# Kernel optimization log

Hardware: AMD Instinct MI355X
Metric: run time of the kernel (lower is better)

Reference implementation:

```python
import jax, jax.numpy as jnp
import numpy as np
import math

SEQ = 45000
FEAT = 30
DEPTH, HEADS, DK, MLP, C = 4, 4, 32, 512, 32
MAXSEQ = 512


def pos_embed_table():
    # Enformer-style basis functions over distances [-SEQ+1, SEQ-1]
    d = jnp.arange(-SEQ + 1, SEQ, dtype=jnp.float32)
    a = jnp.abs(d)[:, None]
    nb = FEAT // 6  # basis per class (exponential / central-mask / gamma)
    # exponential decay
    hl = 2.0 ** jnp.linspace(3.0, math.log(SEQ) / math.log(2.0), nb)
    e1 = jnp.exp(-math.log(2.0) / hl[None, :] * a)
    # central mask
    cw = 2.0 ** jnp.arange(1, nb + 1, dtype=jnp.float32) - 1.0
    e2 = (cw[None, :] > a).astype(jnp.float32)
    # gamma pdf
    stddev = SEQ / (2 * nb)
    start_mean = SEQ / nb
    mean = jnp.linspace(start_mean, float(SEQ), nb)
    conc = (mean / stddev) ** 2
    rate = mean / stddev ** 2
    logp = jax.scipy.special.xlogy(conc - 1.0, a) - rate * a
    logz = jax.scipy.special.gammaln(conc) - conc * jnp.log(rate)
    p = jnp.exp(logp - logz) + 1e-8
    e3 = p / jnp.max(p)
    e = jnp.concatenate([e1, e2, e3], axis=-1)
    return jnp.concatenate([e, jnp.sign(d)[:, None] * e], axis=-1)  # [2*SEQ-1, FEAT]


def layernorm(x, g, b, eps=1e-5):
    mu = jnp.mean(x, axis=-1, keepdims=True)
    var = jnp.var(x, axis=-1, keepdims=True)
    return (x - mu) * jax.lax.rsqrt(var + eps) * g + b


def setup_inputs() -> dict:
    key = jax.random.key(0)
    ks = jax.random.split(key, 16)
    B, L = 2, SEQ
    HD = HEADS * DK
    s = 0.02
    return {
        "x_skip": jax.random.normal(ks[0], (B, C, L), jnp.float32),
        "attention": jax.random.uniform(ks[1], (B, 3, L), jnp.float32),
        "ln1_g": jnp.ones((DEPTH, C), jnp.float32),
        "ln1_b": jnp.zeros((DEPTH, C), jnp.float32),
        "Wq": jax.random.normal(ks[2], (DEPTH, C, HD), jnp.float32) * s,
        "Wk": jax.random.normal(ks[3], (DEPTH, C, HD), jnp.float32) * s,
        "Wv": jax.random.normal(ks[4], (DEPTH, C, HD), jnp.float32) * s,
        "Wrel": jax.random.normal(ks[5], (DEPTH, FEAT, HD), jnp.float32) * s,
        "rcb": jax.random.normal(ks[6], (DEPTH, HEADS, DK), jnp.float32),
        "rpb": jax.random.normal(ks[7], (DEPTH, HEADS, DK), jnp.float32),
        "Wo": jax.random.normal(ks[8], (DEPTH, HD, C), jnp.float32) * s,
        "bo": jnp.zeros((DEPTH, C), jnp.float32),
        "ln2_g": jnp.ones((DEPTH, C), jnp.float32),
        "ln2_b": jnp.zeros((DEPTH, C), jnp.float32),
        "W1": jax.random.normal(ks[9], (DEPTH, C, MLP), jnp.float32) * s,
        "b1": jnp.zeros((DEPTH, MLP), jnp.float32),
        "W2": jax.random.normal(ks[10], (DEPTH, MLP, C), jnp.float32) * s,
        "b2": jnp.zeros((DEPTH, C), jnp.float32),
    }


def reference(x_skip, attention, ln1_g, ln1_b, Wq, Wk, Wv, Wrel, rcb, rpb, Wo, bo, ln2_g, ln2_b, W1, b1, W2, b2):
    B, Cc, L = x_skip.shape
    half = MAXSEQ // 2
    x_emb = jnp.swapaxes(x_skip, 1, 2)  # [B, L, C]
    # top splice sites by acceptor / donor score
    acc = jnp.argsort(-attention[:, 1, :], axis=1)[:, :half]
    don = jnp.argsort(-attention[:, 2, :], axis=1)[:, :half]
    idx = jnp.sort(jnp.concatenate([acc, don], axis=1), axis=1)  # [B, n]
    n = idx.shape[1]
    diff = idx[:, :, None] - idx[:, None, :] + SEQ - 1  # [B, n, n]
    positions = pos_embed_table()[diff]  # [B, n, n, FEAT]
    emb = jnp.take_along_axis(x_emb, idx[:, :, None], axis=1)  # [B, n, C]
    scale = DK ** -0.5
    for l in range(DEPTH):
        h = layernorm(emb, ln1_g[l], ln1_b[l])
        q = (h @ Wq[l]).reshape(B, n, HEADS, DK).transpose(0, 2, 1, 3) * scale
        k = (h @ Wk[l]).reshape(B, n, HEADS, DK).transpose(0, 2, 1, 3)
        v = (h @ Wv[l]).reshape(B, n, HEADS, DK).transpose(0, 2, 1, 3)
        content = jnp.einsum('bhid,bhjd->bhij', q + rcb[l][None, :, None, :], k)
        rel_k = (positions @ Wrel[l]).reshape(B, n, n, HEADS, DK)  # b i j h d
        rel = jnp.einsum('bhid,bijhd->bhij', q + rpb[l][None, :, None, :], rel_k)
        attn_w = jax.nn.softmax(content + rel, axis=-1)
        o = jnp.einsum('bhij,bhjd->bhid', attn_w, v)
        o = o.transpose(0, 2, 1, 3).reshape(B, n, HEADS * DK)
        emb = emb + o @ Wo[l] + bo[l]
        h2 = layernorm(emb, ln2_g[l], ln2_b[l])
        emb = emb + jax.nn.gelu(h2 @ W1[l] + b1[l], approximate=False) @ W2[l] + b2[l]
    out = jnp.zeros_like(x_emb).at[jnp.arange(B)[:, None], idx].set(emb)
    return jnp.swapaxes(out, 1, 2)  # [B, C, L]
```

## Files before the change

kernel.cpp:

```cpp
#include <hip/hip_runtime.h>
#include <math.h>

#define SEQL   45000
#define NBAT   2
#define CCH    32
#define NSEL   512
#define NHEAD  4
#define DKD    32
#define HDD    128
#define MLPD   512
#define CDCAP  2048
#define TKB    32
#define ETB    176

__device__ __forceinline__ unsigned short f2bf(float x) {
  unsigned u = __float_as_uint(x);
  u = (u + 0x7fffu + ((u >> 16) & 1u)) >> 16;
  return (unsigned short)u;
}
#define BFL(u) __uint_as_float((u) << 16)
#define BFH(u) __uint_as_float((u) & 0xffff0000u)
#define U8F(w, s) ((float)(((w) >> (s)) & 0xffu))

__global__ __launch_bounds__(256) void prep_kernel(const float* __restrict__ att,
                                                   unsigned char* __restrict__ E,
                                                   int* __restrict__ hist,
                                                   float* __restrict__ out) {
  {
    int nthr = gridDim.x * 256;
    int gt = blockIdx.x * 256 + threadIdx.x;
    float4 z4 = make_float4(0.f, 0.f, 0.f, 0.f);
    float4* o4 = (float4*)out;
    for (int i = gt; i < NBAT * CCH * SEQL / 4; i += nthr) o4[i] = z4;
  }
  if (blockIdx.x < ETB) {
    int a = blockIdx.x * 256 + threadIdx.x;
    if (a >= SEQL) return;
    float ad = (float)a;
    float outv[16];
    float log2S = log2f((float)SEQL);
    #pragma unroll
    for (int k = 0; k < 5; ++k) {
      float hl = exp2f(3.0f + (float)k * (log2S - 3.0f) * 0.25f);
      outv[k] = exp2f(-ad / hl);
    }
    const int cw[5] = {1, 3, 7, 15, 31};
    #pragma unroll
    for (int k = 0; k < 5; ++k) outv[5 + k] = (a < cw[k]) ? 1.0f : 0.0f;
    float pmax = 0.0f;
    float pk[5];
    #pragma unroll
    for (int k = 0; k < 5; ++k) {
      float mean = 9000.0f * (float)(k + 1);
      float sd = 4500.0f;
      float cc = (mean / sd) * (mean / sd);
      float rr = mean / (sd * sd);
      float logz = lgammaf(cc) - cc * logf(rr);
      float pp;
      if (a == 0) pp = 1e-8f;
      else pp = expf((cc - 1.0f) * logf(ad) - rr * ad - logz) + 1e-8f;
      pk[k] = pp;
      float mstar = (cc - 1.0f) / rr;
      float m0 = floorf(mstar), m1 = m0 + 1.0f;
      if (m1 > (float)(SEQL - 1)) m1 = (float)(SEQL - 1);
      float p0 = expf((cc - 1.0f) * logf(m0) - rr * m0 - logz) + 1e-8f;
      float p1 = expf((cc - 1.0f) * logf(m1) - rr * m1 - logz) + 1e-8f;
      pmax = fmaxf(pmax, fmaxf(p0, p1));
    }
    #pragma unroll
    for (int k = 0; k < 5; ++k) outv[10 + k] = pk[k] / pmax;
    outv[15] = 0.0f;
    unsigned by[16];
    #pragma unroll
    for (int k = 0; k < 15; ++k)
      by[k] = (unsigned)(fminf(fmaxf(outv[k], 0.f), 1.f) * 255.f + 0.5f);
    by[15] = 0u;
    uint4 o;
    o.x = by[0]  | (by[1]  << 8) | (by[2]  << 16) | (by[3]  << 24);
    o.y = by[4]  | (by[5]  << 8) | (by[6]  << 16) | (by[7]  << 24);
    o.z = by[8]  | (by[9]  << 8) | (by[10] << 16) | (by[11] << 24);
    o.w = by[12] | (by[13] << 8) | (by[14] << 16);
    *(uint4*)(E + (size_t)a * 16) = o;
  } else {
    int bid = blockIdx.x - ETB;
    int ch4 = bid / TKB;
    int blk = bid % TKB;
    int b = ch4 >> 1, ch = ch4 & 1;
    const float* row = att + ((size_t)b * 3 + 1 + ch) * SEQL;
    int* h = hist + (size_t)ch4 * 65536;
    int per = (SEQL + TKB - 1) / TKB;
    int lo = blk * per;
    int hi = lo + per; if (hi > SEQL) hi = SEQL;
    for (int i = lo + threadIdx.x; i < hi; i += 256)
      atomicAdd(&h[__float_as_uint(row[i]) >> 16], 1);
  }
}

__global__ __launch_bounds__(256) void topk_collect_kernel(
    const float* __restrict__ att, const int* __restrict__ hist,
    unsigned long long* __restrict__ cand, int* __restrict__ cnt) {
  __shared__ int s_scan[256];
  __shared__ int s_aux[2];
  int tid = threadIdx.x;
  int ch4 = blockIdx.x / TKB;
  int blk = blockIdx.x % TKB;
  const int* h = hist + (size_t)ch4 * 65536;
  {
    int base = tid * 256;
    int sum = 0;
    for (int i = 0; i < 64; ++i) {
      int4 v = ((const int4*)(h + base))[i];
      sum += v.x + v.y + v.z + v.w;
    }
    s_scan[tid] = sum;
  }
  __syncthreads();
  for (int d = 1; d < 256; d <<= 1) {
    int v = s_scan[tid] + ((tid + d < 256) ? s_scan[tid + d] : 0);
    __syncthreads();
    s_scan[tid] = v;
    __syncthreads();
  }
  {
    int sufEx = (tid == 255) ? 0 : s_scan[tid + 1];
    if (s_scan[tid] >= 256 && sufEx < 256) { s_aux[0] = tid; s_aux[1] = 256 - sufEx; }
  }
  __syncthreads();
  int chunk = s_aux[0], want = s_aux[1];
  s_scan[tid] = h[chunk * 256 + tid];
  __syncthreads();
  for (int d = 1; d < 256; d <<= 1) {
    int v = s_scan[tid] + ((tid + d < 256) ? s_scan[tid + d] : 0);
    __syncthreads();
    s_scan[tid] = v;
    __syncthreads();
  }
  {
    int sufEx2 = (tid == 255) ? 0 : s_scan[tid + 1];
    if (s_scan[tid] >= want && sufEx2 < want) s_aux[0] = chunk * 256 + tid;
  }
  __syncthreads();
  unsigned T16 = (unsigned)s_aux[0];
  int b = ch4 >> 1, ch = ch4 & 1;
  const float* row = att + ((size_t)b * 3 + 1 + ch) * SEQL;
  int per = (SEQL + TKB - 1) / TKB;
  int lo = blk * per;
  int hi = lo + per; if (hi > SEQL) hi = SEQL;
  for (int i = lo + tid; i < hi; i += 256) {
    unsigned key = __float_as_uint(row[i]);
    if ((key >> 16) >= T16) {
      int p = atomicAdd(&cnt[ch4], 1);
      if (p < CDCAP)
        cand[(size_t)ch4 * CDCAP + p] =
            ((unsigned long long)key << 32) | (unsigned)(~(unsigned)i);
    }
  }
}

__global__ __launch_bounds__(1024) void topk_sort_kernel(
    const unsigned long long* __restrict__ cand, const int* __restrict__ cnt,
    unsigned* __restrict__ chsel) {
  __shared__ unsigned long long sc[CDCAP];
  int ch4 = blockIdx.x, t = threadIdx.x;
  int n = cnt[ch4]; if (n > CDCAP) n = CDCAP;
  int P = 256;
  while (P < n) P <<= 1;
  for (int i = t; i < P; i += 1024)
    sc[i] = (i < n) ? cand[(size_t)ch4 * CDCAP + i] : 0ull;
  __syncthreads();
  for (int k = 2; k <= P; k <<= 1) {
    for (int j = k >> 1; j > 0; j >>= 1) {
      for (int i = t; i < P; i += 1024) {
        int ixj = i ^ j;
        if (ixj > i) {
          unsigned long long va = sc[i], vb2 = sc[ixj];
          bool up = ((i & k) == 0);
          if ((va < vb2) == up) { sc[i] = vb2; sc[ixj] = va; }
        }
      }
      __syncthreads();
    }
  }
  if (t < 256)
    chsel[(size_t)ch4 * 256 + t] = ~(unsigned)(sc[t] & 0xFFFFFFFFull);
}

__global__ __launch_bounds__(512) void topk_merge_kernel(const unsigned* __restrict__ chsel,
                                                         int* __restrict__ idx) {
  __shared__ int m[512];
  int b = blockIdx.x, tid = threadIdx.x;
  m[tid] = (int)chsel[(size_t)b * 512 + tid];
  __syncthreads();
  for (int k = 2; k <= 512; k <<= 1) {
    for (int j = k >> 1; j > 0; j >>= 1) {
      int ixj = tid ^ j;
      if (ixj > tid) {
        int va = m[tid], vb2 = m[ixj];
        bool up = ((tid & k) == 0);
        if ((va > vb2) == up) { m[tid] = vb2; m[ixj] = va; }
      }
      __syncthreads();
    }
  }
  idx[b * 512 + tid] = m[tid];
}

__global__ __launch_bounds__(128) void gqkv0_kernel(
    const float* __restrict__ x, const int* __restrict__ idx,
    const float* __restrict__ ln_g, const float* __restrict__ ln_b,
    const float* __restrict__ Wq, const float* __restrict__ Wk,
    const float* __restrict__ Wv, const float* __restrict__ Wrel,
    const float* __restrict__ rcb, const float* __restrict__ rpb,
    float* __restrict__ emb, float* __restrict__ qc,
    unsigned short* __restrict__ kbT, unsigned short* __restrict__ vT,
    float* __restrict__ wb) {
  __shared__ float qs[128];
  const int l = 0;
  int hd = threadIdx.x;
  int hh = hd >> 5, d = hd & 31;
  int row = blockIdx.x;
  int b = row >> 9, ii = row & 511;
  int li = idx[b * NSEL + ii];
  float h[32];
  float mu = 0.f;
  #pragma unroll
  for (int c = 0; c < 32; ++c) {
    h[c] = x[((size_t)b * CCH + c) * SEQL + li];
    mu += h[c];
  }
  if (hd < 32) emb[(size_t)row * CCH + hd] = h[hd];
  mu *= (1.0f / 32.0f);
  float var = 0.f;
  #pragma unroll
  for (int c = 0; c < 32; ++c) { float dd0 = h[c] - mu; var += dd0 * dd0; }
  var *= (1.0f / 32.0f);
  float rstd = rsqrtf(var + 1e-5f);
  const float* g = ln_g + l * CCH;
  const float* bb = ln_b + l * CCH;
  #pragma unroll
  for (int c = 0; c < 32; ++c) h[c] = (h[c] - mu) * rstd * g[c] + bb[c];
  const float* wq = Wq + (size_t)l * CCH * HDD + hd;
  const float* wk = Wk + (size_t)l * CCH * HDD + hd;
  const float* wv = Wv + (size_t)l * CCH * HDD + hd;
  float q = 0.f, kk = 0.f, vv = 0.f;
  #pragma unroll
  for (int c = 0; c < 32; ++c) {
    q += h[c] * wq[c * HDD];
    kk += h[c] * wk[c * HDD];
    vv += h[c] * wv[c * HDD];
  }
  q *= 0.17677669529663687f;
  qs[hd] = q;
  qc[(size_t)row * HDD + hd] = q + rcb[(l * NHEAD + hh) * DKD + d];
  size_t tpos = ((size_t)(b * 4 + hh) * 4 + (d >> 3)) * 4096 + (size_t)ii * 8 + (d & 7);
  kbT[tpos] = f2bf(kk);
  vT[tpos]  = f2bf(vv);
  __syncthreads();
  if (hd < 120) {
    int h2 = hd / 30, f = hd % 30;
    const float* wr = Wrel + ((size_t)l * 30 + f) * HDD + h2 * DKD;
    const float* rp = rpb + (l * NHEAD + h2) * DKD;
    const float* qsh = qs + h2 * DKD;
    float acc = 0.f;
    #pragma unroll
    for (int dd = 0; dd < 32; ++dd) acc += (qsh[dd] + rp[dd]) * wr[dd];
    wb[((size_t)row * NHEAD + h2) * 32 + f] = acc;
  }
}

__global__ __launch_bounds__(256, 4) void layer_kernel(
    const float* __restrict__ qc, const unsigned short* __restrict__ kbT,
    const unsigned short* __restrict__ vT, const float* __restrict__ wbuf,
    const unsigned char* __restrict__ E, const int* __restrict__ idx,
    const float* __restrict__ Wo, const float* __restrict__ bo,
    const float* __restrict__ ln2_g, const float* __restrict__ ln2_b,
    const float* __restrict__ W1, const float* __restrict__ b1,
    const float* __restrict__ W2, const float* __restrict__ b2,
    const float* __restrict__ ln1_g, const float* __restrict__ ln1_b,
    const float* __restrict__ Wq, const float* __restrict__ Wk,
    const float* __restrict__ Wv, const float* __restrict__ Wrel,
    const float* __restrict__ rcb, const float* __restrict__ rpb,
    float* __restrict__ emb, float* __restrict__ qcN,
    unsigned short* __restrict__ kbTN, unsigned short* __restrict__ vTN,
    float* __restrict__ wbN, float* __restrict__ out, int layer) {
  __shared__ float es[16 * 512];
  __shared__ float obs[128];
  __shared__ float part[8][32];
  __shared__ float res[32];
  __shared__ float hln[32];
  __shared__ float fin[32];
  __shared__ float a1s[MLPD];
  __shared__ float qs[128];
  int bid = blockIdx.x;
  int b = bid >> 9;
  int i = bid & 511;
  int tid = threadIdx.x;
  int pos = idx[b * NSEL + i];
  #pragma unroll
  for (int rep = 0; rep < 2; ++rep) {
    int j = tid + rep * 256;
    int dj = pos - idx[b * NSEL + j];
    int a = dj < 0 ? -dj : dj;
    uint4 e = *(const uint4*)(E + (size_t)a * 16);
    es[0  * 512 + j] = U8F(e.x, 0);
    es[1  * 512 + j] = U8F(e.x, 8);
    es[2  * 512 + j] = U8F(e.x, 16);
    es[3  * 512 + j] = U8F(e.x, 24);
    es[4  * 512 + j] = U8F(e.y, 0);
    es[5  * 512 + j] = U8F(e.y, 8);
    es[6  * 512 + j] = U8F(e.y, 16);
    es[7  * 512 + j] = U8F(e.y, 24);
    es[8  * 512 + j] = U8F(e.z, 0);
    es[9  * 512 + j] = U8F(e.z, 8);
    es[10 * 512 + j] = U8F(e.z, 16);
    es[11 * 512 + j] = U8F(e.z, 24);
    es[12 * 512 + j] = U8F(e.w, 0);
    es[13 * 512 + j] = U8F(e.w, 8);
    es[14 * 512 + j] = U8F(e.w, 16);
    es[15 * 512 + j] = dj > 0 ? 1.f : (dj < 0 ? -1.f : 0.f);
  }
  __syncthreads();
  {
    int h = tid >> 6, ln = tid & 63;
    const float* qrow = qc + (size_t)(b * NSEL + i) * HDD + h * DKD;
    float q[32];
    #pragma unroll
    for (int d4 = 0; d4 < 8; ++d4) {
      float4 qv = *(const float4*)(qrow + d4 * 4);
      q[d4 * 4 + 0] = qv.x; q[d4 * 4 + 1] = qv.y;
      q[d4 * 4 + 2] = qv.z; q[d4 * 4 + 3] = qv.w;
    }
    const float* wrow = wbuf + ((size_t)(b * NSEL + i) * NHEAD + h) * 32;
    float w0[15], w1[15];
    #pragma unroll
    for (int f = 0; f < 15; ++f) {
      w0[f] = wrow[f] * (1.0f / 255.0f);
      w1[f] = wrow[15 + f] * (1.0f / 255.0f);
    }
    const uint4* kb4 = (const uint4*)kbT + (size_t)(b * 4 + h) * 4 * 512;
    const uint4* vb4 = (const uint4*)vT + (size_t)(b * 4 + h) * 4 * 512;
    float lg[8];
    #pragma unroll
    for (int u = 0; u < 8; ++u) {
      int j = u * 64 + ln;
      float cacc = 0.f;
      #pragma unroll
      for (int dp = 0; dp < 4; ++dp) {
        uint4 kv = kb4[dp * 512 + j];
        cacc += q[dp * 8 + 0] * BFL(kv.x) + q[dp * 8 + 1] * BFH(kv.x)
              + q[dp * 8 + 2] * BFL(kv.y) + q[dp * 8 + 3] * BFH(kv.y)
              + q[dp * 8 + 4] * BFL(kv.z) + q[dp * 8 + 5] * BFH(kv.z)
              + q[dp * 8 + 6] * BFL(kv.w) + q[dp * 8 + 7] * BFH(kv.w);
      }
      float r0 = 0.f, r1 = 0.f;
      #pragma unroll
      for (int f = 0; f < 15; ++f) {
        float ef = es[f * 512 + j];
        r0 += ef * w0[f];
        r1 += ef * w1[f];
      }
      lg[u] = cacc + r0 + es[15 * 512 + j] * r1;
    }
    float m = lg[0];
    #pragma unroll
    for (int u = 1; u < 8; ++u) m = fmaxf(m, lg[u]);
    #pragma unroll
    for (int s = 1; s < 64; s <<= 1) m = fmaxf(m, __shfl_xor(m, s));
    float ssum = 0.f;
    #pragma unroll
    for (int u = 0; u < 8; ++u) { lg[u] = __expf(lg[u] - m); ssum += lg[u]; }
    #pragma unroll
    for (int s = 1; s < 64; s <<= 1) ssum += __shfl_xor(ssum, s);
    float invs = 1.0f / ssum;
    #pragma unroll
    for (int dp = 0; dp < 4; ++dp) {
      float acc[8] = {0.f, 0.f, 0.f, 0.f, 0.f, 0.f, 0.f, 0.f};
      #pragma unroll
      for (int u = 0; u < 8; ++u) {
        uint4 vv = vb4[dp * 512 + u * 64 + ln];
        float p = lg[u];
        acc[0] += p * BFL(vv.x); acc[1] += p * BFH(vv.x);
        acc[2] += p * BFL(vv.y); acc[3] += p * BFH(vv.y);
        acc[4] += p * BFL(vv.z); acc[5] += p * BFH(vv.z);
        acc[6] += p * BFL(vv.w); acc[7] += p * BFH(vv.w);
      }
      #pragma unroll
      for (int s = 1; s < 8; s <<= 1) {
        #pragma unroll
        for (int t = 0; t < 8; ++t) acc[t] += __shfl_xor(acc[t], s);
      }
      int sel = ln & 7;
      float y = acc[0];
      #pragma unroll
      for (int t = 1; t < 8; ++t) y = (sel == t) ? acc[t] : y;
      #pragma unroll
      for (int s = 8; s < 64; s <<= 1) y += __shfl_xor(y, s);
      if (ln < 8) obs[h * DKD + dp * 8 + ln] = y * invs;
    }
  }
  __syncthreads();
  int c = tid & 31, seg = tid >> 5;
  {
    const float* wo = Wo + (size_t)layer * HDD * CCH + c;
    float pacc = 0.f;
    #pragma unroll
    for (int k = 0; k < 16; ++k) {
      int kk = seg * 16 + k;
      pacc += obs[kk] * wo[kk * CCH];
    }
    part[seg][c] = pacc;
  }
  __syncthreads();
  if (tid < 32) {
    float s = bo[layer * CCH + tid] + emb[(size_t)bid * CCH + tid];
    #pragma unroll
    for (int sg = 0; sg < 8; ++sg) s += part[sg][tid];
    res[tid] = s;
  }
  __syncthreads();
  if (tid < 32) {
    float mu = 0.f, s2 = 0.f;
    #pragma unroll
    for (int c2 = 0; c2 < 32; ++c2) { float v = res[c2]; mu += v; s2 += v * v; }
    mu *= (1.0f / 32.0f);
    float var = s2 * (1.0f / 32.0f) - mu * mu;
    float rstd = rsqrtf(var + 1e-5f);
    hln[tid] = (res[tid] - mu) * rstd * ln2_g[layer * CCH + tid] + ln2_b[layer * CCH + tid];
  }
  __syncthreads();
  {
    const float* w1 = W1 + (size_t)layer * CCH * MLPD;
    float accA = b1[layer * MLPD + tid];
    float accB = b1[layer * MLPD + tid + 256];
    for (int c2 = 0; c2 < 32; ++c2) {
      float hv = hln[c2];
      accA += hv * w1[c2 * MLPD + tid];
      accB += hv * w1[c2 * MLPD + tid + 256];
    }
    a1s[tid]       = 0.5f * accA * (1.0f + erff(accA * 0.70710678118654752f));
    a1s[tid + 256] = 0.5f * accB * (1.0f + erff(accB * 0.70710678118654752f));
  }
  __syncthreads();
  {
    const float* w2 = W2 + (size_t)layer * MLPD * CCH;
    float acc2 = 0.f;
    #pragma unroll 4
    for (int mi = 0; mi < 64; ++mi) {
      int m = seg * 64 + mi;
      acc2 += a1s[m] * w2[m * CCH + c];
    }
    __syncthreads();
    part[seg][c] = acc2;
  }
  __syncthreads();
  if (tid < 32) {
    float s = b2[layer * CCH + tid] + res[tid];
    #pragma unroll
    for (int sg = 0; sg < 8; ++sg) s += part[sg][tid];
    fin[tid] = s;
    if (layer < 3) emb[(size_t)bid * CCH + tid] = s;
  }
  __syncthreads();
  if (layer == 3) {
    if (tid < 32) out[((size_t)b * CCH + tid) * SEQL + pos] = fin[tid];
    return;
  }
  const int l1 = layer + 1;
  bool act = tid < 128;
  int hd = tid & 127;
  int hh2 = hd >> 5, dd2 = hd & 31;
  if (act) {
    float hx[32];
    float mu = 0.f;
    #pragma unroll
    for (int c2 = 0; c2 < 32; ++c2) { hx[c2] = fin[c2]; mu += hx[c2]; }
    mu *= (1.0f / 32.0f);
    float var = 0.f;
    #pragma unroll
    for (int c2 = 0; c2 < 32; ++c2) { float dd = hx[c2] - mu; var += dd * dd; }
    var *= (1.0f / 32.0f);
    float rstd = rsqrtf(var + 1e-5f);
    const float* g = ln1_g + l1 * CCH;
    const float* bb = ln1_b + l1 * CCH;
    #pragma unroll
    for (int c2 = 0; c2 < 32; ++c2) hx[c2] = (hx[c2] - mu) * rstd * g[c2] + bb[c2];
    const float* wq = Wq + (size_t)l1 * CCH * HDD + hd;
    const float* wk = Wk + (size_t)l1 * CCH * HDD + hd;
    const float* wv = Wv + (size_t)l1 * CCH * HDD + hd;
    float q = 0.f, kk = 0.f, vv = 0.f;
    #pragma unroll
    for (int c2 = 0; c2 < 32; ++c2) {
      q += hx[c2] * wq[c2 * HDD];
      kk += hx[c2] * wk[c2 * HDD];
      vv += hx[c2] * wv[c2 * HDD];
    }
    q *= 0.17677669529663687f;
    qs[hd] = q;
    qcN[(size_t)bid * HDD + hd] = q + rcb[(l1 * NHEAD + hh2) * DKD + dd2];
    size_t tpos = ((size_t)(b * 4 + hh2) * 4 + (dd2 >> 3)) * 4096 + (size_t)i * 8 + (dd2 & 7);
    kbTN[tpos] = f2bf(kk);
    vTN[tpos]  = f2bf(vv);
  }
  __syncthreads();
  if (act && hd < 120) {
    int h2 = hd / 30, f = hd % 30;
    const float* rp = rpb + (l1 * NHEAD + h2) * DKD;
    const float* wr = Wrel + ((size_t)l1 * 30 + f) * HDD + h2 * DKD;
    const float* qsh = qs + h2 * DKD;
    float acc = 0.f;
    #pragma unroll
    for (int dd = 0; dd < 32; ++dd) acc += (qsh[dd] + rp[dd]) * wr[dd];
    wbN[((size_t)bid * NHEAD + h2) * 32 + f] = acc;
  }
}

extern "C" void kernel_launch(void* const* d_in, const int* in_sizes, int n_in,
                              void* d_out, int out_size, void* d_ws, size_t ws_size,
                              hipStream_t stream) {
  (void)in_sizes; (void)n_in; (void)ws_size; (void)out_size;
  const float* x_skip    = (const float*)d_in[0];
  const float* attention = (const float*)d_in[1];
  const float* ln1_g = (const float*)d_in[2];
  const float* ln1_b = (const float*)d_in[3];
  const float* Wq    = (const float*)d_in[4];
  const float* Wk    = (const float*)d_in[5];
  const float* Wv    = (const float*)d_in[6];
  const float* Wrel  = (const float*)d_in[7];
  const float* rcb   = (const float*)d_in[8];
  const float* rpb   = (const float*)d_in[9];
  const float* Wo    = (const float*)d_in[10];
  const float* bo    = (const float*)d_in[11];
  const float* ln2_g = (const float*)d_in[12];
  const float* ln2_b = (const float*)d_in[13];
  const float* W1    = (const float*)d_in[14];
  const float* b1    = (const float*)d_in[15];
  const float* W2    = (const float*)d_in[16];
  const float* b2    = (const float*)d_in[17];
  float* out = (float*)d_out;
  char* ws = (char*)d_ws;

  unsigned char* E = (unsigned char*)(ws + 0);
  int*      idx   = (int*)(ws + 1441792);
  float*    emb   = (float*)(ws + 1445888);
  float*    qcA   = (float*)(ws + 1576960);
  unsigned short* kbTA = (unsigned short*)(ws + 2101248);
  unsigned short* vTA  = (unsigned short*)(ws + 2363392);
  float*    wbA   = (float*)(ws + 2625536);
  unsigned short* kbTB = (unsigned short*)(ws + 3149824);
  unsigned short* vTB  = (unsigned short*)(ws + 3411968);
  int*      hist  = (int*)(ws + 3674112);
  int*      cnt   = (int*)(ws + 4722688);
  unsigned long long* cand = (unsigned long long*)(ws + 4722720);
  unsigned* chsel = (unsigned*)(ws + 4788256);
  float*    qcB   = (float*)(ws + 4792352);
  float*    wbB   = (float*)(ws + 5316640);

  hipMemsetAsync(ws + 3674112, 0, 1048576 + 32, stream);
  prep_kernel<<<ETB + 4 * TKB, 256, 0, stream>>>(attention, E, hist, out);
  topk_collect_kernel<<<4 * TKB, 256, 0, stream>>>(attention, hist, cand, cnt);
  topk_sort_kernel<<<4, 1024, 0, stream>>>(cand, cnt, chsel);
  topk_merge_kernel<<<2, 512, 0, stream>>>(chsel, idx);
  gqkv0_kernel<<<1024, 128, 0, stream>>>(x_skip, idx, ln1_g, ln1_b, Wq, Wk, Wv,
                                         Wrel, rcb, rpb, emb, qcA, kbTA, vTA, wbA);
  for (int l = 0; l < 4; ++l) {
    const float* qcI = (l & 1) ? qcB : qcA;
    const unsigned short* kbI = (l & 1) ? kbTB : kbTA;
    const unsigned short* vI  = (l & 1) ? vTB : vTA;
    const float* wbI = (l & 1) ? wbB : wbA;
    float* qcO = (l & 1) ? qcA : qcB;
    unsigned short* kbO = (l & 1) ? kbTA : kbTB;
    unsigned short* vO  = (l & 1) ? vTA : vTB;
    float* wbO = (l & 1) ? wbA : wbB;
    layer_kernel<<<1024, 256, 0, stream>>>(qcI, kbI, vI, wbI, E, idx,
                                           Wo, bo, ln2_g, ln2_b, W1, b1, W2, b2,
                                           ln1_g, ln1_b, Wq, Wk, Wv, Wrel, rcb,
                                           rpb, emb, qcO, kbO, vO, wbO, out, l);
  }
}
```

Measured before the change: 306.9 us.

## Split top-k threshold scan, wave-aggregate candidate atomics, fuse sort/merge, pack es as float2

```diff
diff --git a/kernel.cpp b/kernel.cpp
--- a/kernel.cpp
+++ b/kernel.cpp
@@ -96,14 +96,12 @@
   }
 }
 
-__global__ __launch_bounds__(256) void topk_collect_kernel(
-    const float* __restrict__ att, const int* __restrict__ hist,
-    unsigned long long* __restrict__ cand, int* __restrict__ cnt) {
+__global__ __launch_bounds__(256) void topk_thresh_kernel(
+    const int* __restrict__ hist, unsigned* __restrict__ thr) {
   __shared__ int s_scan[256];
   __shared__ int s_aux[2];
   int tid = threadIdx.x;
-  int ch4 = blockIdx.x / TKB;
-  int blk = blockIdx.x % TKB;
+  int ch4 = blockIdx.x;
   const int* h = hist + (size_t)ch4 * 65536;
   {
     int base = tid * 256;
@@ -137,72 +135,92 @@
   }
   {
     int sufEx2 = (tid == 255) ? 0 : s_scan[tid + 1];
-    if (s_scan[tid] >= want && sufEx2 < want) s_aux[0] = chunk * 256 + tid;
-  }
-  __syncthreads();
-  unsigned T16 = (unsigned)s_aux[0];
+    if (s_scan[tid] >= want && sufEx2 < want) thr[ch4] = (unsigned)(chunk * 256 + tid);
+  }
+}
+
+__global__ __launch_bounds__(256) void topk_collect_kernel(
+    const float* __restrict__ att, const unsigned* __restrict__ thr,
+    unsigned long long* __restrict__ cand, int* __restrict__ cnt) {
+  int tid = threadIdx.x;
+  int ch4 = blockIdx.x / TKB;
+  int blk = blockIdx.x % TKB;
+  unsigned T16 = thr[ch4];
   int b = ch4 >> 1, ch = ch4 & 1;
   const float* row = att + ((size_t)b * 3 + 1 + ch) * SEQL;
   int per = (SEQL + TKB - 1) / TKB;
   int lo = blk * per;
   int hi = lo + per; if (hi > SEQL) hi = SEQL;
-  for (int i = lo + tid; i < hi; i += 256) {
-    unsigned key = __float_as_uint(row[i]);
-    if ((key >> 16) >= T16) {
-      int p = atomicAdd(&cnt[ch4], 1);
-      if (p < CDCAP)
-        cand[(size_t)ch4 * CDCAP + p] =
-            ((unsigned long long)key << 32) | (unsigned)(~(unsigned)i);
-    }
-  }
-}
-
-__global__ __launch_bounds__(1024) void topk_sort_kernel(
+  int lane = tid & 63;
+  for (int base = lo; base < hi; base += 256) {
+    int i = base + tid;
+    bool pass = false; unsigned key = 0;
+    if (i < hi) {
+      key = __float_as_uint(row[i]);
+      pass = (key >> 16) >= T16;
+    }
+    unsigned long long mask = __ballot(pass);
+    if (mask) {
+      int np = __popcll(mask);
+      int lead = __ffsll((long long)mask) - 1;
+      int pbase = 0;
+      if (lane == lead) pbase = atomicAdd(&cnt[ch4], np);
+      pbase = __shfl(pbase, lead);
+      if (pass) {
+        int off = __popcll(mask & ((1ull << lane) - 1ull));
+        int p = pbase + off;
+        if (p < CDCAP)
+          cand[(size_t)ch4 * CDCAP + p] =
+              ((unsigned long long)key << 32) | (unsigned)(~(unsigned)i);
+      }
+    }
+  }
+}
+
+__global__ __launch_bounds__(1024) void topk_sortmerge_kernel(
     const unsigned long long* __restrict__ cand, const int* __restrict__ cnt,
-    unsigned* __restrict__ chsel) {
+    int* __restrict__ idx) {
   __shared__ unsigned long long sc[CDCAP];
-  int ch4 = blockIdx.x, t = threadIdx.x;
-  int n = cnt[ch4]; if (n > CDCAP) n = CDCAP;
-  int P = 256;
-  while (P < n) P <<= 1;
-  for (int i = t; i < P; i += 1024)
-    sc[i] = (i < n) ? cand[(size_t)ch4 * CDCAP + i] : 0ull;
-  __syncthreads();
-  for (int k = 2; k <= P; k <<= 1) {
-    for (int j = k >> 1; j > 0; j >>= 1) {
-      for (int i = t; i < P; i += 1024) {
-        int ixj = i ^ j;
-        if (ixj > i) {
-          unsigned long long va = sc[i], vb2 = sc[ixj];
-          bool up = ((i & k) == 0);
-          if ((va < vb2) == up) { sc[i] = vb2; sc[ixj] = va; }
+  __shared__ int m[512];
+  int b = blockIdx.x, t = threadIdx.x;
+  for (int ch = 0; ch < 2; ++ch) {
+    int ch4 = b * 2 + ch;
+    int n = cnt[ch4]; if (n > CDCAP) n = CDCAP;
+    int P = 256;
+    while (P < n) P <<= 1;
+    for (int i = t; i < P; i += 1024)
+      sc[i] = (i < n) ? cand[(size_t)ch4 * CDCAP + i] : 0ull;
+    __syncthreads();
+    for (int k = 2; k <= P; k <<= 1) {
+      for (int j = k >> 1; j > 0; j >>= 1) {
+        for (int i = t; i < P; i += 1024) {
+          int ixj = i ^ j;
+          if (ixj > i) {
+            unsigned long long va = sc[i], vb2 = sc[ixj];
+            bool up = ((i & k) == 0);
+            if ((va < vb2) == up) { sc[i] = vb2; sc[ixj] = va; }
+          }
         }
-      }
-      __syncthreads();
-    }
-  }
-  if (t < 256)
-    chsel[(size_t)ch4 * 256 + t] = ~(unsigned)(sc[t] & 0xFFFFFFFFull);
-}
-
-__global__ __launch_bounds__(512) void topk_merge_kernel(const unsigned* __restrict__ chsel,
-                                                         int* __restrict__ idx) {
-  __shared__ int m[512];
-  int b = blockIdx.x, tid = threadIdx.x;
-  m[tid] = (int)chsel[(size_t)b * 512 + tid];
-  __syncthreads();
+        __syncthreads();
+      }
+    }
+    if (t < 256) m[ch * 256 + t] = (int)~(unsigned)(sc[t] & 0xFFFFFFFFull);
+    __syncthreads();
+  }
   for (int k = 2; k <= 512; k <<= 1) {
     for (int j = k >> 1; j > 0; j >>= 1) {
-      int ixj = tid ^ j;
-      if (ixj > tid) {
-        int va = m[tid], vb2 = m[ixj];
-        bool up = ((tid & k) == 0);
-        if ((va > vb2) == up) { m[tid] = vb2; m[ixj] = va; }
+      if (t < 512) {
+        int ixj = t ^ j;
+        if (ixj > t) {
+          int va = m[t], vb2 = m[ixj];
+          bool up = ((t & k) == 0);
+          if ((va > vb2) == up) { m[t] = vb2; m[ixj] = va; }
+        }
       }
       __syncthreads();
     }
   }
-  idx[b * 512 + tid] = m[tid];
+  if (t < 512) idx[b * 512 + t] = m[t];
 }
 
 __global__ __launch_bounds__(128) void gqkv0_kernel(
@@ -283,7 +301,7 @@
     float* __restrict__ emb, float* __restrict__ qcN,
     unsigned short* __restrict__ kbTN, unsigned short* __restrict__ vTN,
     float* __restrict__ wbN, float* __restrict__ out, int layer) {
-  __shared__ float es[16 * 512];
+  __shared__ float2 es2[8 * 512];
   __shared__ float obs[128];
   __shared__ float part[8][32];
   __shared__ float res[32];
@@ -302,22 +320,15 @@
     int dj = pos - idx[b * NSEL + j];
     int a = dj < 0 ? -dj : dj;
     uint4 e = *(const uint4*)(E + (size_t)a * 16);
-    es[0  * 512 + j] = U8F(e.x, 0);
-    es[1  * 512 + j] = U8F(e.x, 8);
-    es[2  * 512 + j] = U8F(e.x, 16);
-    es[3  * 512 + j] = U8F(e.x, 24);
-    es[4  * 512 + j] = U8F(e.y, 0);
-    es[5  * 512 + j] = U8F(e.y, 8);
-    es[6  * 512 + j] = U8F(e.y, 16);
-    es[7  * 512 + j] = U8F(e.y, 24);
-    es[8  * 512 + j] = U8F(e.z, 0);
-    es[9  * 512 + j] = U8F(e.z, 8);
-    es[10 * 512 + j] = U8F(e.z, 16);
-    es[11 * 512 + j] = U8F(e.z, 24);
-    es[12 * 512 + j] = U8F(e.w, 0);
-    es[13 * 512 + j] = U8F(e.w, 8);
-    es[14 * 512 + j] = U8F(e.w, 16);
-    es[15 * 512 + j] = dj > 0 ? 1.f : (dj < 0 ? -1.f : 0.f);
+    float sgn = dj > 0 ? 1.f : (dj < 0 ? -1.f : 0.f);
+    es2[0 * 512 + j] = make_float2(U8F(e.x, 0),  U8F(e.x, 8));
+    es2[1 * 512 + j] = make_float2(U8F(e.x, 16), U8F(e.x, 24));
+    es2[2 * 512 + j] = make_float2(U8F(e.y, 0),  U8F(e.y, 8));
+    es2[3 * 512 + j] = make_float2(U8F(e.y, 16), U8F(e.y, 24));
+    es2[4 * 512 + j] = make_float2(U8F(e.z, 0),  U8F(e.z, 8));
+    es2[5 * 512 + j] = make_float2(U8F(e.z, 16), U8F(e.z, 24));
+    es2[6 * 512 + j] = make_float2(U8F(e.w, 0),  U8F(e.w, 8));
+    es2[7 * 512 + j] = make_float2(U8F(e.w, 16), sgn);
   }
   __syncthreads();
   {
@@ -353,13 +364,16 @@
               + q[dp * 8 + 6] * BFL(kv.w) + q[dp * 8 + 7] * BFH(kv.w);
       }
       float r0 = 0.f, r1 = 0.f;
+      float2 e7 = es2[7 * 512 + j];
       #pragma unroll
-      for (int f = 0; f < 15; ++f) {
-        float ef = es[f * 512 + j];
-        r0 += ef * w0[f];
-        r1 += ef * w1[f];
-      }
-      lg[u] = cacc + r0 + es[15 * 512 + j] * r1;
+      for (int f2 = 0; f2 < 7; ++f2) {
+        float2 ee = es2[f2 * 512 + j];
+        r0 += ee.x * w0[2 * f2] + ee.y * w0[2 * f2 + 1];
+        r1 += ee.x * w1[2 * f2] + ee.y * w1[2 * f2 + 1];
+      }
+      r0 += e7.x * w0[14];
+      r1 += e7.x * w1[14];
+      lg[u] = cacc + r0 + e7.y * r1;
     }
     float m = lg[0];
     #pragma unroll
@@ -551,15 +565,15 @@
   int*      hist  = (int*)(ws + 3674112);
   int*      cnt   = (int*)(ws + 4722688);
   unsigned long long* cand = (unsigned long long*)(ws + 4722720);
-  unsigned* chsel = (unsigned*)(ws + 4788256);
+  unsigned* thr   = (unsigned*)(ws + 4788256);
   float*    qcB   = (float*)(ws + 4792352);
   float*    wbB   = (float*)(ws + 5316640);
 
   hipMemsetAsync(ws + 3674112, 0, 1048576 + 32, stream);
   prep_kernel<<<ETB + 4 * TKB, 256, 0, stream>>>(attention, E, hist, out);
-  topk_collect_kernel<<<4 * TKB, 256, 0, stream>>>(attention, hist, cand, cnt);
-  topk_sort_kernel<<<4, 1024, 0, stream>>>(cand, cnt, chsel);
-  topk_merge_kernel<<<2, 512, 0, stream>>>(chsel, idx);
+  topk_thresh_kernel<<<4, 256, 0, stream>>>(hist, thr);
+  topk_collect_kernel<<<4 * TKB, 256, 0, stream>>>(attention, thr, cand, cnt);
+  topk_sortmerge_kernel<<<2, 1024, 0, stream>>>(cand, cnt, idx);
   gqkv0_kernel<<<1024, 128, 0, stream>>>(x_skip, idx, ln1_g, ln1_b, Wq, Wk, Wv,
                                          Wrel, rcb, rpb, emb, qcA, kbTA, vTA, wbA);
   for (int l = 0; l < 4; ++l) {
```

New measurement: 320.0 us. +4.3%, slower.

## Fuse top-k histogram, collect and sort into one per-channel kernel

Applied to the files above, without the earlier changes.

```diff
diff --git a/kernel.cpp b/kernel.cpp
--- a/kernel.cpp
+++ b/kernel.cpp
@@ -10,7 +10,6 @@
 #define HDD    128
 #define MLPD   512
 #define CDCAP  2048
-#define TKB    32
 #define ETB    176
 
 __device__ __forceinline__ unsigned short f2bf(float x) {
@@ -22,9 +21,7 @@
 #define BFH(u) __uint_as_float((u) & 0xffff0000u)
 #define U8F(w, s) ((float)(((w) >> (s)) & 0xffu))
 
-__global__ __launch_bounds__(256) void prep_kernel(const float* __restrict__ att,
-                                                   unsigned char* __restrict__ E,
-                                                   int* __restrict__ hist,
+__global__ __launch_bounds__(256) void prep_kernel(unsigned char* __restrict__ E,
                                                    float* __restrict__ out) {
   {
     int nthr = gridDim.x * 256;
@@ -33,149 +30,132 @@
     float4* o4 = (float4*)out;
     for (int i = gt; i < NBAT * CCH * SEQL / 4; i += nthr) o4[i] = z4;
   }
-  if (blockIdx.x < ETB) {
-    int a = blockIdx.x * 256 + threadIdx.x;
-    if (a >= SEQL) return;
-    float ad = (float)a;
-    float outv[16];
-    float log2S = log2f((float)SEQL);
-    #pragma unroll
-    for (int k = 0; k < 5; ++k) {
-      float hl = exp2f(3.0f + (float)k * (log2S - 3.0f) * 0.25f);
-      outv[k] = exp2f(-ad / hl);
-    }
-    const int cw[5] = {1, 3, 7, 15, 31};
-    #pragma unroll
-    for (int k = 0; k < 5; ++k) outv[5 + k] = (a < cw[k]) ? 1.0f : 0.0f;
-    float pmax = 0.0f;
-    float pk[5];
-    #pragma unroll
-    for (int k = 0; k < 5; ++k) {
-      float mean = 9000.0f * (float)(k + 1);
-      float sd = 4500.0f;
-      float cc = (mean / sd) * (mean / sd);
-      float rr = mean / (sd * sd);
-      float logz = lgammaf(cc) - cc * logf(rr);
-      float pp;
-      if (a == 0) pp = 1e-8f;
-      else pp = expf((cc - 1.0f) * logf(ad) - rr * ad - logz) + 1e-8f;
-      pk[k] = pp;
-      float mstar = (cc - 1.0f) / rr;
-      float m0 = floorf(mstar), m1 = m0 + 1.0f;
-      if (m1 > (float)(SEQL - 1)) m1 = (float)(SEQL - 1);
-      float p0 = expf((cc - 1.0f) * logf(m0) - rr * m0 - logz) + 1e-8f;
-      float p1 = expf((cc - 1.0f) * logf(m1) - rr * m1 - logz) + 1e-8f;
-      pmax = fmaxf(pmax, fmaxf(p0, p1));
-    }
-    #pragma unroll
-    for (int k = 0; k < 5; ++k) outv[10 + k] = pk[k] / pmax;
-    outv[15] = 0.0f;
-    unsigned by[16];
-    #pragma unroll
-    for (int k = 0; k < 15; ++k)
-      by[k] = (unsigned)(fminf(fmaxf(outv[k], 0.f), 1.f) * 255.f + 0.5f);
-    by[15] = 0u;
-    uint4 o;
-    o.x = by[0]  | (by[1]  << 8) | (by[2]  << 16) | (by[3]  << 24);
-    o.y = by[4]  | (by[5]  << 8) | (by[6]  << 16) | (by[7]  << 24);
-    o.z = by[8]  | (by[9]  << 8) | (by[10] << 16) | (by[11] << 24);
-    o.w = by[12] | (by[13] << 8) | (by[14] << 16);
-    *(uint4*)(E + (size_t)a * 16) = o;
-  } else {
-    int bid = blockIdx.x - ETB;
-    int ch4 = bid / TKB;
-    int blk = bid % TKB;
-    int b = ch4 >> 1, ch = ch4 & 1;
-    const float* row = att + ((size_t)b * 3 + 1 + ch) * SEQL;
-    int* h = hist + (size_t)ch4 * 65536;
-    int per = (SEQL + TKB - 1) / TKB;
-    int lo = blk * per;
-    int hi = lo + per; if (hi > SEQL) hi = SEQL;
-    for (int i = lo + threadIdx.x; i < hi; i += 256)
-      atomicAdd(&h[__float_as_uint(row[i]) >> 16], 1);
-  }
-}
-
-__global__ __launch_bounds__(256) void topk_collect_kernel(
-    const float* __restrict__ att, const int* __restrict__ hist,
-    unsigned long long* __restrict__ cand, int* __restrict__ cnt) {
-  __shared__ int s_scan[256];
-  __shared__ int s_aux[2];
-  int tid = threadIdx.x;
-  int ch4 = blockIdx.x / TKB;
-  int blk = blockIdx.x % TKB;
-  const int* h = hist + (size_t)ch4 * 65536;
-  {
-    int base = tid * 256;
-    int sum = 0;
-    for (int i = 0; i < 64; ++i) {
-      int4 v = ((const int4*)(h + base))[i];
-      sum += v.x + v.y + v.z + v.w;
-    }
-    s_scan[tid] = sum;
-  }
-  __syncthreads();
-  for (int d = 1; d < 256; d <<= 1) {
-    int v = s_scan[tid] + ((tid + d < 256) ? s_scan[tid + d] : 0);
-    __syncthreads();
-    s_scan[tid] = v;
-    __syncthreads();
-  }
-  {
-    int sufEx = (tid == 255) ? 0 : s_scan[tid + 1];
-    if (s_scan[tid] >= 256 && sufEx < 256) { s_aux[0] = tid; s_aux[1] = 256 - sufEx; }
-  }
-  __syncthreads();
-  int chunk = s_aux[0], want = s_aux[1];
-  s_scan[tid] = h[chunk * 256 + tid];
-  __syncthreads();
-  for (int d = 1; d < 256; d <<= 1) {
-    int v = s_scan[tid] + ((tid + d < 256) ? s_scan[tid + d] : 0);
-    __syncthreads();
-    s_scan[tid] = v;
-    __syncthreads();
-  }
-  {
-    int sufEx2 = (tid == 255) ? 0 : s_scan[tid + 1];
-    if (s_scan[tid] >= want && sufEx2 < want) s_aux[0] = chunk * 256 + tid;
-  }
-  __syncthreads();
-  unsigned T16 = (unsigned)s_aux[0];
+  if (blockIdx.x >= ETB) return;
+  int a = blockIdx.x * 256 + threadIdx.x;
+  if (a >= SEQL) return;
+  float ad = (float)a;
+  float outv[16];
+  float log2S = log2f((float)SEQL);
+  #pragma unroll
+  for (int k = 0; k < 5; ++k) {
+    float hl = exp2f(3.0f + (float)k * (log2S - 3.0f) * 0.25f);
+    outv[k] = exp2f(-ad / hl);
+  }
+  const int cw[5] = {1, 3, 7, 15, 31};
+  #pragma unroll
+  for (int k = 0; k < 5; ++k) outv[5 + k] = (a < cw[k]) ? 1.0f : 0.0f;
+  float pmax = 0.0f;
+  float pk[5];
+  #pragma unroll
+  for (int k = 0; k < 5; ++k) {
+    float mean = 9000.0f * (float)(k + 1);
+    float sd = 4500.0f;
+    float cc = (mean / sd) * (mean / sd);
+    float rr = mean / (sd * sd);
+    float logz = lgammaf(cc) - cc * logf(rr);
+    float pp;
+    if (a == 0) pp = 1e-8f;
+    else pp = expf((cc - 1.0f) * logf(ad) - rr * ad - logz) + 1e-8f;
+    pk[k] = pp;
+    float mstar = (cc - 1.0f) / rr;
+    float m0 = floorf(mstar), m1 = m0 + 1.0f;
+    if (m1 > (float)(SEQL - 1)) m1 = (float)(SEQL - 1);
+    float p0 = expf((cc - 1.0f) * logf(m0) - rr * m0 - logz) + 1e-8f;
+    float p1 = expf((cc - 1.0f) * logf(m1) - rr * m1 - logz) + 1e-8f;
+    pmax = fmaxf(pmax, fmaxf(p0, p1));
+  }
+  #pragma unroll
+  for (int k = 0; k < 5; ++k) outv[10 + k] = pk[k] / pmax;
+  outv[15] = 0.0f;
+  unsigned by[16];
+  #pragma unroll
+  for (int k = 0; k < 15; ++k)
+    by[k] = (unsigned)(fminf(fmaxf(outv[k], 0.f), 1.f) * 255.f + 0.5f);
+  by[15] = 0u;
+  uint4 o;
+  o.x = by[0]  | (by[1]  << 8) | (by[2]  << 16) | (by[3]  << 24);
+  o.y = by[4]  | (by[5]  << 8) | (by[6]  << 16) | (by[7]  << 24);
+  o.z = by[8]  | (by[9]  << 8) | (by[10] << 16) | (by[11] << 24);
+  o.w = by[12] | (by[13] << 8) | (by[14] << 16);
+  *(uint4*)(E + (size_t)a * 16) = o;
+}
+
+__global__ __launch_bounds__(1024) void topk_channel_kernel(
+    const float* __restrict__ att, unsigned* __restrict__ chsel) {
+  __shared__ unsigned long long sc[CDCAP];
+  __shared__ int hist[256];
+  __shared__ int scan[256];
+  __shared__ int aux[2];
+  __shared__ int cnt;
+  int ch4 = blockIdx.x, t = threadIdx.x;
   int b = ch4 >> 1, ch = ch4 & 1;
   const float* row = att + ((size_t)b * 3 + 1 + ch) * SEQL;
-  int per = (SEQL + TKB - 1) / TKB;
-  int lo = blk * per;
-  int hi = lo + per; if (hi > SEQL) hi = SEQL;
-  for (int i = lo + tid; i < hi; i += 256) {
+  if (t < 256) hist[t] = 0;
+  if (t == 0) cnt = 0;
+  __syncthreads();
+  for (int i = t; i < SEQL; i += 1024)
+    atomicAdd(&hist[__float_as_uint(row[i]) >> 24], 1);
+  __syncthreads();
+  if (t < 256) scan[t] = hist[t];
+  __syncthreads();
+  for (int d = 1; d < 256; d <<= 1) {
+    int v = 0;
+    if (t < 256) v = scan[t] + ((t + d < 256) ? scan[t + d] : 0);
+    __syncthreads();
+    if (t < 256) scan[t] = v;
+    __syncthreads();
+  }
+  if (t < 256) {
+    int sufEx = (t == 255) ? 0 : scan[t + 1];
+    if (scan[t] >= 256 && sufEx < 256) { aux[0] = t; aux[1] = 256 - sufEx; }
+  }
+  __syncthreads();
+  int B = aux[0], want = aux[1];
+  if (t < 256) hist[t] = 0;
+  __syncthreads();
+  for (int i = t; i < SEQL; i += 1024) {
+    unsigned key = __float_as_uint(row[i]);
+    if ((int)(key >> 24) == B) atomicAdd(&hist[(key >> 16) & 0xffu], 1);
+  }
+  __syncthreads();
+  if (t < 256) scan[t] = hist[t];
+  __syncthreads();
+  for (int d = 1; d < 256; d <<= 1) {
+    int v = 0;
+    if (t < 256) v = scan[t] + ((t + d < 256) ? scan[t + d] : 0);
+    __syncthreads();
+    if (t < 256) scan[t] = v;
+    __syncthreads();
+  }
+  if (t < 256) {
+    int sufEx = (t == 255) ? 0 : scan[t + 1];
+    if (scan[t] >= want && sufEx < want) aux[0] = (B << 8) | t;
+  }
+  __syncthreads();
+  unsigned T16 = (unsigned)aux[0];
+  for (int i = t; i < SEQL; i += 1024) {
     unsigned key = __float_as_uint(row[i]);
     if ((key >> 16) >= T16) {
-      int p = atomicAdd(&cnt[ch4], 1);
+      int p = atomicAdd(&cnt, 1);
       if (p < CDCAP)
-        cand[(size_t)ch4 * CDCAP + p] =
-            ((unsigned long long)key << 32) | (unsigned)(~(unsigned)i);
-    }
-  }
-}
-
-__global__ __launch_bounds__(1024) void topk_sort_kernel(
-    const unsigned long long* __restrict__ cand, const int* __restrict__ cnt,
-    unsigned* __restrict__ chsel) {
-  __shared__ unsigned long long sc[CDCAP];
-  int ch4 = blockIdx.x, t = threadIdx.x;
-  int n = cnt[ch4]; if (n > CDCAP) n = CDCAP;
+        sc[p] = ((unsigned long long)key << 32) | (unsigned)(~(unsigned)i);
+    }
+  }
+  __syncthreads();
+  int n = cnt; if (n > CDCAP) n = CDCAP;
   int P = 256;
   while (P < n) P <<= 1;
-  for (int i = t; i < P; i += 1024)
-    sc[i] = (i < n) ? cand[(size_t)ch4 * CDCAP + i] : 0ull;
+  for (int i2 = t; i2 < P; i2 += 1024)
+    if (i2 >= n) sc[i2] = 0ull;
   __syncthreads();
   for (int k = 2; k <= P; k <<= 1) {
     for (int j = k >> 1; j > 0; j >>= 1) {
-      for (int i = t; i < P; i += 1024) {
-        int ixj = i ^ j;
-        if (ixj > i) {
-          unsigned long long va = sc[i], vb2 = sc[ixj];
-          bool up = ((i & k) == 0);
-          if ((va < vb2) == up) { sc[i] = vb2; sc[ixj] = va; }
+      for (int i2 = t; i2 < P; i2 += 1024) {
+        int ixj = i2 ^ j;
+        if (ixj > i2) {
+          unsigned long long va = sc[i2], vb2 = sc[ixj];
+          bool up = ((i2 & k) == 0);
+          if ((va < vb2) == up) { sc[i2] = vb2; sc[ixj] = va; }
         }
       }
       __syncthreads();
@@ -283,7 +263,7 @@
     float* __restrict__ emb, float* __restrict__ qcN,
     unsigned short* __restrict__ kbTN, unsigned short* __restrict__ vTN,
     float* __restrict__ wbN, float* __restrict__ out, int layer) {
-  __shared__ float es[16 * 512];
+  __shared__ float2 es2[8 * 512];
   __shared__ float obs[128];
   __shared__ float part[8][32];
   __shared__ float res[32];
@@ -302,22 +282,15 @@
     int dj = pos - idx[b * NSEL + j];
     int a = dj < 0 ? -dj : dj;
     uint4 e = *(const uint4*)(E + (size_t)a * 16);
-    es[0  * 512 + j] = U8F(e.x, 0);
-    es[1  * 512 + j] = U8F(e.x, 8);
-    es[2  * 512 + j] = U8F(e.x, 16);
-    es[3  * 512 + j] = U8F(e.x, 24);
-    es[4  * 512 + j] = U8F(e.y, 0);
-    es[5  * 512 + j] = U8F(e.y, 8);
-    es[6  * 512 + j] = U8F(e.y, 16);
-    es[7  * 512 + j] = U8F(e.y, 24);
-    es[8  * 512 + j] = U8F(e.z, 0);
-    es[9  * 512 + j] = U8F(e.z, 8);
-    es[10 * 512 + j] = U8F(e.z, 16);
-    es[11 * 512 + j] = U8F(e.z, 24);
-    es[12 * 512 + j] = U8F(e.w, 0);
-    es[13 * 512 + j] = U8F(e.w, 8);
-    es[14 * 512 + j] = U8F(e.w, 16);
-    es[15 * 512 + j] = dj > 0 ? 1.f : (dj < 0 ? -1.f : 0.f);
+    float sgn = dj > 0 ? 1.f : (dj < 0 ? -1.f : 0.f);
+    es2[0 * 512 + j] = make_float2(U8F(e.x, 0),  U8F(e.x, 8));
+    es2[1 * 512 + j] = make_float2(U8F(e.x, 16), U8F(e.x, 24));
+    es2[2 * 512 + j] = make_float2(U8F(e.y, 0),  U8F(e.y, 8));
+    es2[3 * 512 + j] = make_float2(U8F(e.y, 16), U8F(e.y, 24));
+    es2[4 * 512 + j] = make_float2(U8F(e.z, 0),  U8F(e.z, 8));
+    es2[5 * 512 + j] = make_float2(U8F(e.z, 16), U8F(e.z, 24));
+    es2[6 * 512 + j] = make_float2(U8F(e.w, 0),  U8F(e.w, 8));
+    es2[7 * 512 + j] = make_float2(U8F(e.w, 16), sgn);
   }
   __syncthreads();
   {
@@ -353,13 +326,16 @@
               + q[dp * 8 + 6] * BFL(kv.w) + q[dp * 8 + 7] * BFH(kv.w);
       }
       float r0 = 0.f, r1 = 0.f;
+      float2 e7 = es2[7 * 512 + j];
       #pragma unroll
-      for (int f = 0; f < 15; ++f) {
-        float ef = es[f * 512 + j];
-        r0 += ef * w0[f];
-        r1 += ef * w1[f];
+      for (int f2 = 0; f2 < 7; ++f2) {
+        float2 ee = es2[f2 * 512 + j];
+        r0 += ee.x * w0[2 * f2] + ee.y * w0[2 * f2 + 1];
+        r1 += ee.x * w1[2 * f2] + ee.y * w1[2 * f2 + 1];
       }
-      lg[u] = cacc + r0 + es[15 * 512 + j] * r1;
+      r0 += e7.x * w0[14];
+      r1 += e7.x * w1[14];
+      lg[u] = cacc + r0 + e7.y * r1;
     }
     float m = lg[0];
     #pragma unroll
@@ -548,17 +524,12 @@
   float*    wbA   = (float*)(ws + 2625536);
   unsigned short* kbTB = (unsigned short*)(ws + 3149824);
   unsigned short* vTB  = (unsigned short*)(ws + 3411968);
-  int*      hist  = (int*)(ws + 3674112);
-  int*      cnt   = (int*)(ws + 4722688);
-  unsigned long long* cand = (unsigned long long*)(ws + 4722720);
   unsigned* chsel = (unsigned*)(ws + 4788256);
   float*    qcB   = (float*)(ws + 4792352);
   float*    wbB   = (float*)(ws + 5316640);
 
-  hipMemsetAsync(ws + 3674112, 0, 1048576 + 32, stream);
-  prep_kernel<<<ETB + 4 * TKB, 256, 0, stream>>>(attention, E, hist, out);
-  topk_collect_kernel<<<4 * TKB, 256, 0, stream>>>(attention, hist, cand, cnt);
-  topk_sort_kernel<<<4, 1024, 0, stream>>>(cand, cnt, chsel);
+  prep_kernel<<<ETB + 128, 256, 0, stream>>>(attention ? E : E, out);
+  topk_channel_kernel<<<4, 1024, 0, stream>>>(attention, chsel);
   topk_merge_kernel<<<2, 512, 0, stream>>>(chsel, idx);
   gqkv0_kernel<<<1024, 128, 0, stream>>>(x_skip, idx, ln1_g, ln1_b, Wq, Wk, Wv,
                                          Wrel, rcb, rpb, emb, qcA, kbTA, vTA, wbA);
```

After: 300.6 us. 2.0% less time.
